# Kernel optimization log

Hardware: AMD Instinct MI355X
Metric: run time of the kernel (lower is better)

Reference implementation:

```python
import jax, jax.numpy as jnp
import numpy as np

B, SQ, SV, D = 4, 4096, 4096, 64


def setup_inputs() -> dict:
    key = jax.random.key(0)
    kq, kv = jax.random.split(key)
    query = jax.random.normal(kq, (B, SQ, D), dtype=jnp.float32)
    value = jax.random.normal(kv, (B, SV, D), dtype=jnp.float32)
    return {"query": query, "value": value}


def reference(query, value):
    # scores: [B, Sq, Sv] = Q @ V^T  (no scale, no mask, as in the original)
    scores = jnp.einsum("bqd,bvd->bqv", query, value)
    weights = jax.nn.softmax(scores, axis=-1)
    # output: [B, Sq, D]
    return jnp.einsum("bqv,bvd->bqd", weights, value)
```

## Files before the change

### kernel.cpp

```cpp
#include <hip/hip_runtime.h>
#include <hip/hip_bf16.h>
#include <stdint.h>

#define BATCH 4
#define SQN   4096
#define SVN   4096
#define DIM   64
#define KT    32
#define NTILE (SVN / KT)
#define NSTEPH 64

#define RMS 72
#define TRS 40
#define IMG_RM_H 0
#define IMG_RM_L 4608
#define IMG_TR_H 9216
#define IMG_TR_L 14336
#define BLOB     19456
#define LDS_BYTES (4 * BLOB)

typedef __attribute__((ext_vector_type(8))) short bf16x8;
typedef __attribute__((ext_vector_type(4))) float f32x4;
typedef __attribute__((ext_vector_type(4))) unsigned int u32x4;

#if __has_builtin(__builtin_amdgcn_exp2f)
#define EXP2F __builtin_amdgcn_exp2f
#else
#define EXP2F exp2f
#endif

static __device__ __forceinline__ unsigned short bf16_rne(float x) {
  unsigned u = __float_as_uint(x);
  u += 0x7FFFu + ((u >> 16) & 1u);
  return (unsigned short)(u >> 16);
}
static __device__ __forceinline__ float bf16f(unsigned short h) {
  return __uint_as_float((unsigned)h << 16);
}
static __device__ __forceinline__ unsigned cvt_pk_bf16(float lo, float hi) {
  unsigned r;
  asm("v_cvt_pk_bf16_f32 %0, %1, %2" : "=v"(r) : "v"(lo), "v"(hi));
  return r;
}

__global__ __launch_bounds__(256) void vprep_kernel(const float* __restrict__ V,
                                                    char* __restrict__ ws) {
  __shared__ unsigned ex[32][65];
  const int b    = blockIdx.x >> 7;
  const int tile = blockIdx.x & 127;
  const int t    = threadIdx.x;
  const int vv   = t >> 3;
  const int d0   = (t & 7) * 8;

  const float* src = V + (((size_t)b * SVN + (size_t)tile * KT + vv) * DIM + d0);
  const float4 a0 = ((const float4*)src)[0];
  const float4 a1 = ((const float4*)src)[1];
  const float x[8] = {a0.x, a0.y, a0.z, a0.w, a1.x, a1.y, a1.z, a1.w};

  unsigned short h[8], l[8];
#pragma unroll
  for (int j = 0; j < 8; ++j) {
    h[j] = bf16_rne(x[j]);
    l[j] = bf16_rne(x[j] - bf16f(h[j]));
  }

  char* blob = ws + (size_t)(b * NTILE + tile) * BLOB;

  const int p = (((vv >> 2) & 1) << 4) | ((vv >> 3) << 2) | (vv & 3);
  bf16x8 vh, vl;
#pragma unroll
  for (int j = 0; j < 8; ++j) { vh[j] = (short)h[j]; vl[j] = (short)l[j]; }
  *(bf16x8*)(blob + IMG_RM_H + (p * RMS + d0) * 2) = vh;
  *(bf16x8*)(blob + IMG_RM_L + (p * RMS + d0) * 2) = vl;

#pragma unroll
  for (int j = 0; j < 8; ++j) ex[vv][d0 + j] = (unsigned)h[j] | ((unsigned)l[j] << 16);
  __syncthreads();

  const int r  = t >> 1;
  const int pl = r >> 6;
  const int d  = r & 63;
  const int hh = t & 1;
  unsigned w16[16];
#pragma unroll
  for (int c = 0; c < 16; ++c) w16[c] = ex[hh * 16 + c][d];
  u32x4 o0, o1;
#pragma unroll
  for (int k = 0; k < 8; ++k) {
    const unsigned w0 = w16[2 * k], w1 = w16[2 * k + 1];
    const unsigned dw = pl ? ((w0 >> 16) | (w1 & 0xFFFF0000u))
                           : ((w0 & 0xFFFFu) | (w1 << 16));
    if (k < 4) o0[k] = dw; else o1[k - 4] = dw;
  }
  char* dst = blob + (pl ? IMG_TR_L : IMG_TR_H) + (d * TRS + hh * 16) * 2;
  ((u32x4*)dst)[0] = o0;
  ((u32x4*)dst)[1] = o1;
}

__global__ __launch_bounds__(256, 2) void attn_kernel(const float* __restrict__ Qg,
                                                      const char* __restrict__ vprep,
                                                      float* __restrict__ out) {
  extern __shared__ char smem[];
  const int raw = blockIdx.x;
  const int lb = (raw & 7) * 32 + (raw >> 3);
  const int batch = lb >> 6;
  const int qbase = (lb & 63) * 64;
  const int tid = threadIdx.x;
  const int lane = tid & 63;
  const int wid = tid >> 6;
  const int qt = wid & 1;
  const int half = wid >> 1;
  const int lr = lane & 15;
  const int lg = lane >> 4;

  bf16x8 Qh[2][2], Ql[2][2];
#pragma unroll
  for (int qb = 0; qb < 2; ++qb) {
    const size_t qrow = (size_t)batch * SQN + qbase + qt * 32 + qb * 16 + lr;
#pragma unroll
    for (int ks = 0; ks < 2; ++ks) {
      const float* qp = Qg + qrow * DIM + ks * 32 + 8 * lg;
      const float4 f0 = ((const float4*)qp)[0];
      const float4 f1 = ((const float4*)qp)[1];
      const float xv[8] = {f0.x, f0.y, f0.z, f0.w, f1.x, f1.y, f1.z, f1.w};
#pragma unroll
      for (int j = 0; j < 8; ++j) {
        const float v = xv[j] * 1.44269504088896f;
        const unsigned short hh = bf16_rne(v);
        Qh[qb][ks][j] = (short)hh;
        Ql[qb][ks][j] = (short)bf16_rne(v - bf16f(hh));
      }
    }
  }

  f32x4 Oacc[2][4];
#pragma unroll
  for (int qb = 0; qb < 2; ++qb)
#pragma unroll
    for (int db = 0; db < 4; ++db) Oacc[qb][db] = (f32x4){0.f, 0.f, 0.f, 0.f};
  float m_[2] = {-1e30f, -1e30f};
  float l_[2] = {0.f, 0.f};

  const size_t tb0 = (size_t)(batch * NTILE) * BLOB;

  auto stage = [&](int t, int b) {
    const size_t g0 = tb0 + (size_t)(half * NSTEPH + t) * BLOB;
    char* l0 = smem + (half * 2 + b) * BLOB;
    const int c0 = qt * 9;
#pragma unroll
    for (int k = 0; k < 10; ++k) {
      const int sub = c0 + k;
      __builtin_amdgcn_global_load_lds(
          (const __attribute__((address_space(1))) unsigned int*)(vprep + g0 + sub * 1024 + lane * 16),
          (__attribute__((address_space(3))) unsigned int*)(l0 + sub * 1024), 16, 0, 0);
    }
  };

  stage(0, 0);
  int buf = 0;

  for (int t = 0; t < NSTEPH; ++t) {
    asm volatile("s_waitcnt vmcnt(0)" ::: "memory");
    __builtin_amdgcn_s_barrier();
    if (t + 1 < NSTEPH) stage(t + 1, buf ^ 1);

    const char* qbuf = smem + (half * 2 + buf) * BLOB;

    bf16x8 Vh[2][2], Vl[2][2];
#pragma unroll
    for (int vt = 0; vt < 2; ++vt)
#pragma unroll
      for (int ks = 0; ks < 2; ++ks) {
        const int off = ((vt * 16 + lr) * RMS + ks * 32 + 8 * lg) * 2;
        Vh[vt][ks] = *(const bf16x8*)(qbuf + IMG_RM_H + off);
        Vl[vt][ks] = *(const bf16x8*)(qbuf + IMG_RM_L + off);
      }
    bf16x8 Ah[4], Al[4];
#pragma unroll
    for (int db = 0; db < 4; ++db) {
      const int toff = ((db * 16 + lr) * TRS + 8 * lg) * 2;
      Ah[db] = *(const bf16x8*)(qbuf + IMG_TR_H + toff);
      Al[db] = *(const bf16x8*)(qbuf + IMG_TR_L + toff);
    }

    f32x4 sacc[2][2];
    __builtin_amdgcn_s_setprio(1);
#pragma unroll
    for (int qb = 0; qb < 2; ++qb)
#pragma unroll
      for (int vt = 0; vt < 2; ++vt) {
        f32x4 acc = (f32x4){0.f, 0.f, 0.f, 0.f};
#pragma unroll
        for (int ks = 0; ks < 2; ++ks) {
          acc = __builtin_amdgcn_mfma_f32_16x16x32_bf16(Vh[vt][ks], Qh[qb][ks], acc, 0, 0, 0);
          acc = __builtin_amdgcn_mfma_f32_16x16x32_bf16(Vh[vt][ks], Ql[qb][ks], acc, 0, 0, 0);
          acc = __builtin_amdgcn_mfma_f32_16x16x32_bf16(Vl[vt][ks], Qh[qb][ks], acc, 0, 0, 0);
        }
        sacc[qb][vt] = acc;
      }
    __builtin_amdgcn_s_setprio(0);

    bf16x8 Ph[2], Pl[2];
#pragma unroll
    for (int qb = 0; qb < 2; ++qb) {
      float mt = -1e30f;
#pragma unroll
      for (int vt = 0; vt < 2; ++vt)
#pragma unroll
        for (int r = 0; r < 4; ++r) mt = fmaxf(mt, sacc[qb][vt][r]);
      mt = fmaxf(mt, __shfl_xor(mt, 16, 64));
      mt = fmaxf(mt, __shfl_xor(mt, 32, 64));

      float p[8];
      float rs = 0.f;
      if (__any(mt > m_[qb] + 8.0f)) {
        const float mnew = fmaxf(m_[qb], mt);
        const float alpha = EXP2F(m_[qb] - mnew);
#pragma unroll
        for (int vt = 0; vt < 2; ++vt)
#pragma unroll
          for (int r = 0; r < 4; ++r) {
            const float pv = EXP2F(sacc[qb][vt][r] - mnew);
            p[vt * 4 + r] = pv;
            rs += pv;
          }
        rs += __shfl_xor(rs, 16, 64);
        rs += __shfl_xor(rs, 32, 64);
        l_[qb] = l_[qb] * alpha + rs;
        m_[qb] = mnew;
#pragma unroll
        for (int db = 0; db < 4; ++db) Oacc[qb][db] *= alpha;
      } else {
#pragma unroll
        for (int vt = 0; vt < 2; ++vt)
#pragma unroll
          for (int r = 0; r < 4; ++r) {
            const float pv = EXP2F(sacc[qb][vt][r] - m_[qb]);
            p[vt * 4 + r] = pv;
            rs += pv;
          }
        rs += __shfl_xor(rs, 16, 64);
        rs += __shfl_xor(rs, 32, 64);
        l_[qb] += rs;
      }

      u32x4 hu, lu;
#pragma unroll
      for (int j = 0; j < 4; ++j) {
        const unsigned hd = cvt_pk_bf16(p[2 * j], p[2 * j + 1]);
        const float h0 = __uint_as_float(hd << 16);
        const float h1 = __uint_as_float(hd & 0xFFFF0000u);
        hu[j] = hd;
        lu[j] = cvt_pk_bf16(p[2 * j] - h0, p[2 * j + 1] - h1);
      }
      Ph[qb] = __builtin_bit_cast(bf16x8, hu);
      Pl[qb] = __builtin_bit_cast(bf16x8, lu);
    }

    __builtin_amdgcn_s_setprio(1);
#pragma unroll
    for (int db = 0; db < 4; ++db)
#pragma unroll
      for (int qb = 0; qb < 2; ++qb) {
        Oacc[qb][db] = __builtin_amdgcn_mfma_f32_16x16x32_bf16(Ah[db], Ph[qb], Oacc[qb][db], 0, 0, 0);
        Oacc[qb][db] = __builtin_amdgcn_mfma_f32_16x16x32_bf16(Al[db], Ph[qb], Oacc[qb][db], 0, 0, 0);
        Oacc[qb][db] = __builtin_amdgcn_mfma_f32_16x16x32_bf16(Ah[db], Pl[qb], Oacc[qb][db], 0, 0, 0);
      }
    __builtin_amdgcn_s_setprio(0);

    buf ^= 1;
  }

  __syncthreads();

  float* mbuf = (float*)smem;
  float* mlb  = (float*)(smem + 2 * 64 * 68 * 4);
#pragma unroll
  for (int qb = 0; qb < 2; ++qb) {
    const int ridx = half * 64 + qt * 32 + qb * 16 + lr;
    float* dst = mbuf + ridx * 68;
#pragma unroll
    for (int db = 0; db < 4; ++db)
#pragma unroll
      for (int r = 0; r < 4; ++r) dst[db * 16 + 4 * lg + r] = Oacc[qb][db][r];
    if (lg == 0) {
      mlb[ridx * 2 + 0] = m_[qb];
      mlb[ridx * 2 + 1] = l_[qb];
    }
  }
  __syncthreads();

  const int qh = tid >> 3;
  const int d0 = (tid & 7) * 8;
#pragma unroll
  for (int rep = 0; rep < 2; ++rep) {
    const int q = rep * 32 + qh;
    const float M = fmaxf(mlb[q * 2], mlb[(64 + q) * 2]);
    float L = 0.f;
    float o[8] = {0, 0, 0, 0, 0, 0, 0, 0};
#pragma unroll
    for (int hf = 0; hf < 2; ++hf) {
      const int ridx = hf * 64 + q;
      const float a = EXP2F(mlb[ridx * 2] - M);
      L += a * mlb[ridx * 2 + 1];
      const float* srcp = mbuf + ridx * 68 + d0;
#pragma unroll
      for (int j = 0; j < 8; ++j) o[j] += a * srcp[j];
    }
    const float inv = 1.0f / L;
    float* op = out + ((size_t)batch * SQN + qbase + q) * DIM + d0;
    float4 w0 = {o[0] * inv, o[1] * inv, o[2] * inv, o[3] * inv};
    float4 w1 = {o[4] * inv, o[5] * inv, o[6] * inv, o[7] * inv};
    ((float4*)op)[0] = w0;
    ((float4*)op)[1] = w1;
  }
}

extern "C" void kernel_launch(void* const* d_in, const int* in_sizes, int n_in,
                              void* d_out, int out_size, void* d_ws, size_t ws_size,
                              hipStream_t stream) {
  const float* Qg = (const float*)d_in[0];
  const float* Vg = (const float*)d_in[1];
  float* out = (float*)d_out;
  char* ws = (char*)d_ws;
  const size_t need = (size_t)BATCH * NTILE * BLOB;
  if (ws_size < need) return;

  hipFuncSetAttribute((const void*)attn_kernel,
                      hipFuncAttributeMaxDynamicSharedMemorySize, LDS_BYTES);

  vprep_kernel<<<BATCH * NTILE, 256, 0, stream>>>(Vg, ws);
  attn_kernel<<<256, 256, LDS_BYTES, stream>>>(Qg, ws, out);
}
```

Measured before the change: 155.1 us.

## Split key dimension across two blocks and merge partial softmax results

Adds a split-KV variant of the attention kernel: each query block's value sequence is divided between two workgroups, doubling the grid from 256 to 512 blocks. Each block writes unnormalized partial outputs plus running max and sum to workspace, and a separate merge kernel combines them. The aim is to fill more of the MI355X's compute units, since 256 blocks underoccupy the device. The cost is an extra kernel launch and a global round trip for the partial outputs. The split path runs only when the workspace is large enough, otherwise the single-pass path is kept.

```diff
diff --git a/kernel.cpp b/kernel.cpp
--- a/kernel.cpp
+++ b/kernel.cpp
@@ -8,7 +8,6 @@
 #define DIM   64
 #define KT    32
 #define NTILE (SVN / KT)
-#define NSTEPH 64
 
 #define RMS 72
 #define TRS 40
@@ -19,6 +18,10 @@
 #define BLOB     19456
 #define LDS_BYTES (4 * BLOB)
 
+#define BLOB_BYTES ((size_t)BATCH * NTILE * BLOB)
+#define PARTO_ELEMS ((size_t)512 * 64 * 64)
+#define PARTML_ELEMS ((size_t)512 * 64 * 2)
+
 typedef __attribute__((ext_vector_type(8))) short bf16x8;
 typedef __attribute__((ext_vector_type(4))) float f32x4;
 typedef __attribute__((ext_vector_type(4))) unsigned int u32x4;
@@ -97,14 +100,23 @@
   ((u32x4*)dst)[1] = o1;
 }
 
+template <int SPLIT>
 __global__ __launch_bounds__(256, 2) void attn_kernel(const float* __restrict__ Qg,
                                                       const char* __restrict__ vprep,
+                                                      float* __restrict__ partO,
+                                                      float* __restrict__ partML,
                                                       float* __restrict__ out) {
+  constexpr int NSTEP = (SPLIT == 2) ? 32 : 64;
   extern __shared__ char smem[];
   const int raw = blockIdx.x;
-  const int lb = (raw & 7) * 32 + (raw >> 3);
-  const int batch = lb >> 6;
-  const int qbase = (lb & 63) * 64;
+  int batch, qblock, svh;
+  if constexpr (SPLIT == 2) {
+    batch = (raw & 7) >> 1; svh = raw & 1; qblock = raw >> 3;
+  } else {
+    const int lb = (raw & 7) * 32 + (raw >> 3);
+    batch = lb >> 6; qblock = lb & 63; svh = 0;
+  }
+  const int qbase = qblock * 64;
   const int tid = threadIdx.x;
   const int lane = tid & 63;
   const int wid = tid >> 6;
@@ -142,9 +154,10 @@
   float l_[2] = {0.f, 0.f};
 
   const size_t tb0 = (size_t)(batch * NTILE) * BLOB;
+  const int tile0 = svh * 64 + half * NSTEP;
 
   auto stage = [&](int t, int b) {
-    const size_t g0 = tb0 + (size_t)(half * NSTEPH + t) * BLOB;
+    const size_t g0 = tb0 + (size_t)(tile0 + t) * BLOB;
     char* l0 = smem + (half * 2 + b) * BLOB;
     const int c0 = qt * 9;
 #pragma unroll
@@ -159,10 +172,10 @@
   stage(0, 0);
   int buf = 0;
 
-  for (int t = 0; t < NSTEPH; ++t) {
+  for (int t = 0; t < NSTEP; ++t) {
     asm volatile("s_waitcnt vmcnt(0)" ::: "memory");
     __builtin_amdgcn_s_barrier();
-    if (t + 1 < NSTEPH) stage(t + 1, buf ^ 1);
+    if (t + 1 < NSTEP) stage(t + 1, buf ^ 1);
 
     const char* qbuf = smem + (half * 2 + buf) * BLOB;
 
@@ -307,13 +320,61 @@
 #pragma unroll
       for (int j = 0; j < 8; ++j) o[j] += a * srcp[j];
     }
-    const float inv = 1.0f / L;
-    float* op = out + ((size_t)batch * SQN + qbase + q) * DIM + d0;
-    float4 w0 = {o[0] * inv, o[1] * inv, o[2] * inv, o[3] * inv};
-    float4 w1 = {o[4] * inv, o[5] * inv, o[6] * inv, o[7] * inv};
-    ((float4*)op)[0] = w0;
-    ((float4*)op)[1] = w1;
-  }
+    if constexpr (SPLIT == 1) {
+      const float inv = 1.0f / L;
+      float* op = out + ((size_t)batch * SQN + qbase + q) * DIM + d0;
+      float4 w0 = {o[0] * inv, o[1] * inv, o[2] * inv, o[3] * inv};
+      float4 w1 = {o[4] * inv, o[5] * inv, o[6] * inv, o[7] * inv};
+      ((float4*)op)[0] = w0;
+      ((float4*)op)[1] = w1;
+    } else {
+      const int pslot = (batch * 64 + qblock) * 2 + svh;
+      float* po = partO + ((size_t)pslot * 64 + q) * 64 + d0;
+      float4 w0 = {o[0], o[1], o[2], o[3]};
+      float4 w1 = {o[4], o[5], o[6], o[7]};
+      ((float4*)po)[0] = w0;
+      ((float4*)po)[1] = w1;
+      if (d0 == 0) {
+        partML[((size_t)pslot * 64 + q) * 2 + 0] = M;
+        partML[((size_t)pslot * 64 + q) * 2 + 1] = L;
+      }
+    }
+  }
+}
+
+__global__ __launch_bounds__(256) void merge_kernel(const float* __restrict__ partO,
+                                                    const float* __restrict__ partML,
+                                                    float* __restrict__ out) {
+  const int gidx = blockIdx.x * 256 + threadIdx.x;
+  const int pq = gidx >> 3;
+  const int d0 = (gidx & 7) * 8;
+  const int batch = pq >> 12;
+  const int qb = (pq >> 6) & 63;
+  const int qr = pq & 63;
+  const int slot0 = (batch * 64 + qb) * 2;
+
+  const float m0 = partML[((size_t)slot0 * 64 + qr) * 2 + 0];
+  const float l0 = partML[((size_t)slot0 * 64 + qr) * 2 + 1];
+  const float m1 = partML[((size_t)(slot0 + 1) * 64 + qr) * 2 + 0];
+  const float l1 = partML[((size_t)(slot0 + 1) * 64 + qr) * 2 + 1];
+  const float M = fmaxf(m0, m1);
+  const float a0 = EXP2F(m0 - M);
+  const float a1 = EXP2F(m1 - M);
+  const float inv = 1.0f / (a0 * l0 + a1 * l1);
+
+  const float* p0 = partO + ((size_t)slot0 * 64 + qr) * 64 + d0;
+  const float* p1 = partO + ((size_t)(slot0 + 1) * 64 + qr) * 64 + d0;
+  const float4 x0 = ((const float4*)p0)[0];
+  const float4 x1 = ((const float4*)p0)[1];
+  const float4 y0 = ((const float4*)p1)[0];
+  const float4 y1 = ((const float4*)p1)[1];
+  float4 w0 = {(a0 * x0.x + a1 * y0.x) * inv, (a0 * x0.y + a1 * y0.y) * inv,
+               (a0 * x0.z + a1 * y0.z) * inv, (a0 * x0.w + a1 * y0.w) * inv};
+  float4 w1 = {(a0 * x1.x + a1 * y1.x) * inv, (a0 * x1.y + a1 * y1.y) * inv,
+               (a0 * x1.z + a1 * y1.z) * inv, (a0 * x1.w + a1 * y1.w) * inv};
+  float* op = out + (size_t)pq * DIM + d0;
+  ((float4*)op)[0] = w0;
+  ((float4*)op)[1] = w1;
 }
 
 extern "C" void kernel_launch(void* const* d_in, const int* in_sizes, int n_in,
@@ -323,12 +384,23 @@
   const float* Vg = (const float*)d_in[1];
   float* out = (float*)d_out;
   char* ws = (char*)d_ws;
-  const size_t need = (size_t)BATCH * NTILE * BLOB;
-  if (ws_size < need) return;
-
-  hipFuncSetAttribute((const void*)attn_kernel,
-                      hipFuncAttributeMaxDynamicSharedMemorySize, LDS_BYTES);
+
+  const size_t need1 = BLOB_BYTES;
+  const size_t need2 = BLOB_BYTES + (PARTO_ELEMS + PARTML_ELEMS) * 4;
+  if (ws_size < need1) return;
 
   vprep_kernel<<<BATCH * NTILE, 256, 0, stream>>>(Vg, ws);
-  attn_kernel<<<256, 256, LDS_BYTES, stream>>>(Qg, ws, out);
-}
+
+  if (ws_size >= need2) {
+    float* partO  = (float*)(ws + BLOB_BYTES);
+    float* partML = partO + PARTO_ELEMS;
+    hipFuncSetAttribute((const void*)attn_kernel<2>,
+                        hipFuncAttributeMaxDynamicSharedMemorySize, LDS_BYTES);
+    attn_kernel<2><<<512, 256, LDS_BYTES, stream>>>(Qg, ws, partO, partML, out);
+    merge_kernel<<<512, 256, 0, stream>>>(partO, partML, out);
+  } else {
+    hipFuncSetAttribute((const void*)attn_kernel<1>,
+                        hipFuncAttributeMaxDynamicSharedMemorySize, LDS_BYTES);
+    attn_kernel<1><<<256, 256, LDS_BYTES, stream>>>(Qg, ws, nullptr, nullptr, out);
+  }
+}
```

Result: faster. 140.4 us (-9.4%).
